# Kernel optimization log

Measured on AMD Instinct MI355X. Metric: run time of the kernel, lower is better.

The kernel has to match this reference:

```python
import jax, jax.numpy as jnp
import numpy as np
from jax import lax

P = 8  # DFFN patch_size


def _ln(x, w, b):
    # WithBias LayerNorm over channel dim of NCHW (matches to_3d -> LN(-1) -> to_4d)
    mu = x.mean(1, keepdims=True)
    var = ((x - mu) ** 2).mean(1, keepdims=True)
    return (x - mu) / jnp.sqrt(var + 1e-5) * w[None, :, None, None] + b[None, :, None, None]


def _conv1x1(x, w, b=None):
    y = jnp.einsum('bchw,oc->bohw', x, w)
    if b is not None:
        y = y + b[None, :, None, None]
    return y


def setup_inputs() -> dict:
    key = jax.random.key(0)
    ks = jax.random.split(key, 9)
    B, C, H, W = 2, 64, 96, 96
    hid = C  # ffn_expansion_factor = 1
    s = lambda k, shape, scale=0.05: jax.random.normal(k, shape, jnp.float32) * scale
    return {
        'x': s(ks[0], (B, C, H, W), 1.0),
        'ln1_w': jnp.ones((C,), jnp.float32), 'ln1_b': jnp.zeros((C,), jnp.float32),
        'ln2_w': jnp.ones((C,), jnp.float32), 'ln2_b': jnp.zeros((C,), jnp.float32),
        'q_w': s(ks[1], (C, C)), 'q_b': jnp.zeros((C,), jnp.float32),
        'k_w': s(ks[2], (C, C)), 'k_b': jnp.zeros((C,), jnp.float32),
        'v_w': s(ks[3], (C, C)), 'v_b': jnp.zeros((C,), jnp.float32),
        'fft_w': s(ks[4], (hid, P, P // 2 + 1), 1.0),
        'proj_in_w': s(ks[5], (hid, C)),
        'dw_w': s(ks[6], (hid, 1, 3, 3)),
        'proj_out_w': s(ks[7], (C, hid // 2)),
    }


def reference(x, ln1_w, ln1_b, ln2_w, ln2_b, q_w, q_b, k_w, k_b, v_w, v_b,
              fft_w, proj_in_w, dw_w, proj_out_w):
    B, C, H, W = x.shape
    # --- attention sub-block (unscaled spatial self-attn) ---
    xn = _ln(x, ln1_w, ln1_b)
    q = _conv1x1(xn, q_w, q_b).reshape(B, C, H * W)
    k = _conv1x1(xn, k_w, k_b).reshape(B, C, H * W)
    v = _conv1x1(xn, v_w, v_b).reshape(B, C, H * W)
    attn = jax.nn.softmax(jnp.einsum('bcn,bcm->bnm', q, k), axis=-1)  # [B, HW, HW]
    out = jnp.einsum('bcm,bnm->bcn', v, attn).reshape(B, C, H, W)
    x = x + out
    # --- DFFN sub-block ---
    xn = _ln(x, ln2_w, ln2_b)
    h = _conv1x1(xn, proj_in_w)  # hidden == C (expansion factor 1)
    hid = h.shape[1]
    hb, wb = H // P, W // P
    hp = h.reshape(B, hid, hb, P, wb, P).transpose(0, 2, 4, 1, 3, 5)  # [B,hb,wb,hid,P,P]
    hf = jnp.fft.rfft2(hp) * fft_w  # real learned spectral filter
    hp = jnp.fft.irfft2(hf, s=(P, P))
    h = hp.transpose(0, 3, 1, 4, 2, 5).reshape(B, hid, H, W)
    h = lax.conv_general_dilated(h, dw_w, (1, 1), ((1, 1), (1, 1)),
                                 feature_group_count=hid,
                                 dimension_numbers=('NCHW', 'OIHW', 'NCHW'))
    h1, h2 = jnp.split(h, 2, axis=1)
    h = jax.nn.gelu(h1, approximate=False) * h2  # torch F.gelu is exact erf
    return x + _conv1x1(h, proj_out_w)
```

## Files before the change

### kernel.cpp

```cpp
#include <hip/hip_runtime.h>
#include <hip/hip_bf16.h>
#include <math.h>

#define CH 64
#define NPOS 9216
#define NTOT 18432
#define NSPLIT 12
#define TILES_PER_SPLIT 12
#define LOG2E 1.4426950408889634f

typedef short bf16x8 __attribute__((ext_vector_type(8)));
typedef short bf16x4 __attribute__((ext_vector_type(4)));
typedef float f32x4 __attribute__((ext_vector_type(4)));
typedef int   i32x4 __attribute__((ext_vector_type(4)));
typedef int   i32x2 __attribute__((ext_vector_type(2)));
typedef unsigned int u32;

__device__ __forceinline__ float bf2f(short s) {
  unsigned int u = ((unsigned int)(unsigned short)s) << 16;
  return __builtin_bit_cast(float, u);
}
__device__ __forceinline__ short f2bf(float f) {
  unsigned int u = __builtin_bit_cast(unsigned int, f);
  unsigned int r = (u + 0x7fffu + ((u >> 16) & 1u)) >> 16;
  return (short)r;
}
__device__ __forceinline__ float gelu_exact(float x) {
  return 0.5f * x * (1.f + erff(x * 0.70710678118654752440f));
}


__global__ __launch_bounds__(256) void k_ln_qkv(
    const float* __restrict__ x, const float* __restrict__ ln1w, const float* __restrict__ ln1b,
    const float* __restrict__ qw, const float* __restrict__ qb,
    const float* __restrict__ kw, const float* __restrict__ kb,
    const float* __restrict__ vw, const float* __restrict__ vb,
    short* __restrict__ Qg, short* __restrict__ Kg, short* __restrict__ Vgt) {
  __shared__ float s1a[256], s2a[256];
  __shared__ __align__(16) short xn[32 * 72];
  int t = threadIdx.x;
  int w8 = t >> 5;
  int p = t & 31;
  int q0 = blockIdx.x * 32;
  int q = q0 + p;
  int b = q / NPOS;
  int nn = q0 % NPOS;
  int n = q % NPOS;

  const float* xb = x + (size_t)b * CH * NPOS + n;
  float xr[8];
  float s1 = 0.f, s2 = 0.f;
#pragma unroll
  for (int cl = 0; cl < 8; ++cl) {
    float v = xb[(size_t)(w8 * 8 + cl) * NPOS];
    xr[cl] = v;
    s1 += v;
    s2 += v * v;
  }
  s1a[w8 * 32 + p] = s1;
  s2a[w8 * 32 + p] = s2;
  __syncthreads();
  float mu = 0.f, m2 = 0.f;
#pragma unroll
  for (int ww = 0; ww < 8; ++ww) { mu += s1a[ww * 32 + p]; m2 += s2a[ww * 32 + p]; }
  mu *= (1.f / 64.f);
  float var = m2 * (1.f / 64.f) - mu * mu;
  float rstd = rsqrtf(var + 1e-5f);
  {
    u32* xw = (u32*)xn;
#pragma unroll
    for (int j2 = 0; j2 < 4; ++j2) {
      int cl = 2 * j2, c = w8 * 8 + cl;
      float y0 = (xr[cl] - mu) * rstd * ln1w[c] + ln1b[c];
      float y1 = (xr[cl + 1] - mu) * rstd * ln1w[c + 1] + ln1b[c + 1];
      u32 pk = ((u32)(unsigned short)f2bf(y1) << 16) | (u32)(unsigned short)f2bf(y0);
      xw[p * 36 + w8 * 4 + j2] = pk;
    }
  }
  __syncthreads();
  int lane = t & 63;
  int L = lane & 15, quad = lane >> 4;
  int cs = t >> 6;
  bf16x8 b0[2], b1[2];
#pragma unroll
  for (int ps = 0; ps < 2; ++ps) {
    b0[ps] = *(const bf16x8*)(xn + (ps * 16 + L) * 72 + quad * 8);
    b1[ps] = *(const bf16x8*)(xn + (ps * 16 + L) * 72 + 32 + quad * 8);
  }
#pragma unroll
  for (int m = 0; m < 3; ++m) {
    const float* wsrc = (m == 0) ? qw : (m == 1) ? kw : vw;
    const float* bsrc = (m == 0) ? qb : (m == 1) ? kb : vb;
    bf16x8 a0, a1;
    {
      const float* wr = wsrc + (cs * 16 + L) * 64 + quad * 8;
#pragma unroll
      for (int j = 0; j < 8; ++j) { a0[j] = f2bf(wr[j]); a1[j] = f2bf(wr[32 + j]); }
    }
    float bi[4];
#pragma unroll
    for (int i = 0; i < 4; ++i) bi[i] = bsrc[cs * 16 + quad * 4 + i];
#pragma unroll
    for (int ps = 0; ps < 2; ++ps) {
      f32x4 acc = {bi[0], bi[1], bi[2], bi[3]};
      acc = __builtin_amdgcn_mfma_f32_16x16x32_bf16(a0, b0[ps], acc, 0, 0, 0);
      acc = __builtin_amdgcn_mfma_f32_16x16x32_bf16(a1, b1[ps], acc, 0, 0, 0);
      int idx = b * NPOS + nn + ps * 16 + L;
      if (m == 0) {
#pragma unroll
        for (int i = 0; i < 4; ++i)
          Qg[(size_t)idx * 64 + cs * 16 + quad * 4 + i] = f2bf(acc[i]);
      } else if (m == 1) {
#pragma unroll
        for (int i = 0; i < 4; ++i)
          Kg[(size_t)idx * 64 + cs * 16 + quad * 4 + i] = f2bf(acc[i] * LOG2E);
      } else {
#pragma unroll
        for (int i = 0; i < 4; ++i)
          Vgt[(size_t)(cs * 16 + quad * 4 + i) * NTOT + idx] = f2bf(acc[i]);
      }
    }
  }
}

#define LDPK 80
#define LDP  72
__global__ __launch_bounds__(512) void k_attn(
    const short* __restrict__ Qg, const short* __restrict__ Kg, const short* __restrict__ Vgt,
    u32* __restrict__ PoT, float* __restrict__ Pl) {
  __shared__ __align__(16) short Kt[2][64 * LDPK];
  __shared__ __align__(16) short Vt[2][64 * LDP];
  int b = blockIdx.y;
  int n0 = blockIdx.x * 256;
  int ks = blockIdx.z;
  int tid = threadIdx.x;
  int w = tid >> 6, lane = tid & 63;
  int L = lane & 15, quad = lane >> 4;

  bf16x8 qa[2][2];
#pragma unroll
  for (int qt = 0; qt < 2; ++qt) {
    const short* qb_ = Qg + ((size_t)(b * NPOS + n0 + w * 32 + qt * 16 + L)) * 64;
    qa[qt][0] = *(const bf16x8*)(qb_ + quad * 8);
    qa[qt][1] = *(const bf16x8*)(qb_ + 32 + quad * 8);
  }

  f32x4 o[2][4];
#pragma unroll
  for (int qt = 0; qt < 2; ++qt)
#pragma unroll
    for (int nb = 0; nb < 4; ++nb) o[qt][nb] = (f32x4){0.f, 0.f, 0.f, 0.f};
  float rl[2] = {0.f, 0.f};

  int ck = tid & 7, rk = tid >> 3;
  int c8 = tid & 7, dr = tid >> 3;
  int vslot = (c8 >> 2) * 32 + (c8 & 1) * 16 + ((c8 >> 1) & 1) * 4;
  i32x4 kr, vr;
  {
    int kt = ks * TILES_PER_SPLIT;
    kr = ((const i32x4*)(Kg + ((size_t)(b * NPOS + kt * 64)) * 64))[tid];
    vr = *(const i32x4*)(Vgt + (size_t)b * NPOS + kt * 64 + c8 * 8 + (size_t)dr * NTOT);
    ((i32x4*)Kt[0])[rk * 10 + ck] = kr;
    short* vrow = Vt[0] + dr * LDP + vslot;
    *(i32x2*)(vrow) = (i32x2){vr[0], vr[1]};
    *(i32x2*)(vrow + 8) = (i32x2){vr[2], vr[3]};
  }

  for (int t = 0; t < TILES_PER_SPLIT; ++t) {
    int cur = t & 1;
    if (t + 1 < TILES_PER_SPLIT) {
      int kt = ks * TILES_PER_SPLIT + t + 1;
      kr = ((const i32x4*)(Kg + ((size_t)(b * NPOS + kt * 64)) * 64))[tid];
      vr = *(const i32x4*)(Vgt + (size_t)b * NPOS + kt * 64 + c8 * 8 + (size_t)dr * NTOT);
    }
    __syncthreads();

    const i32x4* kt4 = (const i32x4*)Kt[cur];
    const short* vt = Vt[cur];
    auto compute_win = [&](int kp) {
      u32 pw0[4], pw1[4];
#pragma unroll
      for (int h = 0; h < 2; ++h) {
        int kti = kp * 2 + h;
        bf16x8 kf0 = __builtin_bit_cast(bf16x8, kt4[(kti * 16 + L) * 10 + quad]);
        bf16x8 kf1 = __builtin_bit_cast(bf16x8, kt4[(kti * 16 + L) * 10 + 4 + quad]);
#pragma unroll
        for (int qt = 0; qt < 2; ++qt) {
          f32x4 st = {0.f, 0.f, 0.f, 0.f};
          st = __builtin_amdgcn_mfma_f32_16x16x32_bf16(kf0, qa[qt][0], st, 0, 0, 0);
          st = __builtin_amdgcn_mfma_f32_16x16x32_bf16(kf1, qa[qt][1], st, 0, 0, 0);
          float p0 = __builtin_amdgcn_exp2f(st[0]);
          float p1 = __builtin_amdgcn_exp2f(st[1]);
          float p2 = __builtin_amdgcn_exp2f(st[2]);
          float p3 = __builtin_amdgcn_exp2f(st[3]);
          rl[qt] += (p0 + p1) + (p2 + p3);
          u32 lo = __builtin_amdgcn_perm(__builtin_bit_cast(u32, p1), __builtin_bit_cast(u32, p0), 0x07060302u);
          u32 hi = __builtin_amdgcn_perm(__builtin_bit_cast(u32, p3), __builtin_bit_cast(u32, p2), 0x07060302u);
          if (qt == 0) { pw0[h * 2] = lo; pw0[h * 2 + 1] = hi; }
          else         { pw1[h * 2] = lo; pw1[h * 2 + 1] = hi; }
        }
      }
      i32x4 pq0 = {(int)pw0[0], (int)pw0[1], (int)pw0[2], (int)pw0[3]};
      i32x4 pq1 = {(int)pw1[0], (int)pw1[1], (int)pw1[2], (int)pw1[3]};
      bf16x8 pp0 = __builtin_bit_cast(bf16x8, pq0);
      bf16x8 pp1 = __builtin_bit_cast(bf16x8, pq1);
#pragma unroll
      for (int nb = 0; nb < 4; ++nb) {
        bf16x8 va8 = *(const bf16x8*)(vt + (nb * 16 + L) * LDP + kp * 32 + quad * 8);
        o[0][nb] = __builtin_amdgcn_mfma_f32_16x16x32_bf16(va8, pp0, o[0][nb], 0, 0, 0);
        o[1][nb] = __builtin_amdgcn_mfma_f32_16x16x32_bf16(va8, pp1, o[1][nb], 0, 0, 0);
      }
    };

    __builtin_amdgcn_s_setprio(1);
    compute_win(0);
    __builtin_amdgcn_s_setprio(0);

    if (t + 1 < TILES_PER_SPLIT) {
      int nxt = 1 - cur;
      ((i32x4*)Kt[nxt])[rk * 10 + ck] = kr;
      short* vrow = Vt[nxt] + dr * LDP + vslot;
      *(i32x2*)(vrow) = (i32x2){vr[0], vr[1]};
      *(i32x2*)(vrow + 8) = (i32x2){vr[2], vr[3]};
    }

    __builtin_amdgcn_s_setprio(1);
    compute_win(1);
    __builtin_amdgcn_s_setprio(0);
  }

#pragma unroll
  for (int qt = 0; qt < 2; ++qt) {
    rl[qt] += __shfl_xor(rl[qt], 16);
    rl[qt] += __shfl_xor(rl[qt], 32);
  }

#pragma unroll
  for (int qt = 0; qt < 2; ++qt) {
    int qg = b * NPOS + n0 + w * 32 + qt * 16 + L;
#pragma unroll
    for (int nb = 0; nb < 4; ++nb)
#pragma unroll
      for (int ip = 0; ip < 2; ++ip) {
        u32 pk = ((u32)(unsigned short)f2bf(o[qt][nb][2 * ip + 1]) << 16) |
                 (u32)(unsigned short)f2bf(o[qt][nb][2 * ip]);
        int d32 = nb * 8 + quad * 2 + ip;
        PoT[((size_t)(ks * 32 + d32)) * NTOT + qg] = pk;
      }
    if (quad == 0) Pl[(size_t)ks * NTOT + qg] = rl[qt];
  }
}

__global__ __launch_bounds__(256) void k_res_ln2_proj(
    const float* __restrict__ x, const u32* __restrict__ PoT, const float* __restrict__ Pl,
    const float* __restrict__ ln2w, const float* __restrict__ ln2b,
    const float* __restrict__ piw,
    float* __restrict__ X2, float* __restrict__ Hbuf) {
  __shared__ float s1a[32 * 32], s2a[32 * 32];
  __shared__ float inva[32], mua[32], rsa[32];
  __shared__ __align__(16) short xn[32 * 72];
  int t = threadIdx.x;
  int q0 = blockIdx.x * 32;
  int b = q0 / NPOS;
  int nn = q0 % NPOS;

  if (t < 32) {
    float ls = 0.f;
#pragma unroll
    for (int s = 0; s < NSPLIT; ++s) ls += Pl[(size_t)s * NTOT + q0 + t];
    inva[t] = 1.f / ls;
  }
  __syncthreads();

  int rho = t >> 3;
  int p4 = (t & 7) * 4;
  int c0 = rho * 2;

  float aL[4] = {0.f, 0.f, 0.f, 0.f}, aH[4] = {0.f, 0.f, 0.f, 0.f};
#pragma unroll
  for (int s = 0; s < NSPLIT; ++s) {
    i32x4 v = *(const i32x4*)(PoT + (size_t)(s * 32 + rho) * NTOT + q0 + p4);
#pragma unroll
    for (int i = 0; i < 4; ++i) {
      u32 u = (u32)v[i];
      aL[i] += __builtin_bit_cast(float, u << 16);
      aH[i] += __builtin_bit_cast(float, u & 0xffff0000u);
    }
  }
  f32x4 x0 = *(const f32x4*)(x + (size_t)b * CH * NPOS + (size_t)c0 * NPOS + nn + p4);
  f32x4 x1 = *(const f32x4*)(x + (size_t)b * CH * NPOS + (size_t)(c0 + 1) * NPOS + nn + p4);
  float v0[4], v1[4];
  f32x4 ps1, ps2;
#pragma unroll
  for (int i = 0; i < 4; ++i) {
    float iv = inva[p4 + i];
    v0[i] = x0[i] + aL[i] * iv;
    v1[i] = x1[i] + aH[i] * iv;
    ps1[i] = v0[i] + v1[i];
    ps2[i] = v0[i] * v0[i] + v1[i] * v1[i];
  }
  *(f32x4*)&s1a[rho * 32 + p4] = ps1;
  *(f32x4*)&s2a[rho * 32 + p4] = ps2;
  {
    float* xo = X2 + (size_t)b * CH * NPOS + nn + p4;
    *(f32x4*)(xo + (size_t)c0 * NPOS) = (f32x4){v0[0], v0[1], v0[2], v0[3]};
    *(f32x4*)(xo + (size_t)(c0 + 1) * NPOS) = (f32x4){v1[0], v1[1], v1[2], v1[3]};
  }
  __syncthreads();
  if (t < 32) {
    float m = 0.f, m2 = 0.f;
#pragma unroll
    for (int r = 0; r < 32; ++r) { m += s1a[r * 32 + t]; m2 += s2a[r * 32 + t]; }
    m *= (1.f / 64.f);
    float var = m2 * (1.f / 64.f) - m * m;
    mua[t] = m;
    rsa[t] = rsqrtf(var + 1e-5f);
  }
  __syncthreads();
  {
    u32* xw = (u32*)xn;
    float w0 = ln2w[c0], w1 = ln2w[c0 + 1];
    float bb0 = ln2b[c0], bb1 = ln2b[c0 + 1];
#pragma unroll
    for (int i = 0; i < 4; ++i) {
      int p = p4 + i;
      float mu = mua[p], rs = rsa[p];
      float y0 = (v0[i] - mu) * rs * w0 + bb0;
      float y1 = (v1[i] - mu) * rs * w1 + bb1;
      xw[p * 36 + rho] = ((u32)(unsigned short)f2bf(y1) << 16) | (u32)(unsigned short)f2bf(y0);
    }
  }
  __syncthreads();
  int lane = t & 63;
  int L = lane & 15, quad = lane >> 4;
  int cs = t >> 6;
  bf16x8 a0, a1;
  {
    const float* wr = piw + (cs * 16 + L) * 64 + quad * 8;
#pragma unroll
    for (int j = 0; j < 8; ++j) { a0[j] = f2bf(wr[j]); a1[j] = f2bf(wr[32 + j]); }
  }
  float* hb = Hbuf + (size_t)b * CH * NPOS + nn;
#pragma unroll
  for (int ps = 0; ps < 2; ++ps) {
    bf16x8 b0 = *(const bf16x8*)(xn + (ps * 16 + L) * 72 + quad * 8);
    bf16x8 b1 = *(const bf16x8*)(xn + (ps * 16 + L) * 72 + 32 + quad * 8);
    f32x4 acc = {0.f, 0.f, 0.f, 0.f};
    acc = __builtin_amdgcn_mfma_f32_16x16x32_bf16(a0, b0, acc, 0, 0, 0);
    acc = __builtin_amdgcn_mfma_f32_16x16x32_bf16(a1, b1, acc, 0, 0, 0);
#pragma unroll
    for (int i = 0; i < 4; ++i)
      hb[(size_t)(cs * 16 + quad * 4 + i) * NPOS + ps * 16 + L] = acc[i];
  }
}

#define LDB 100
__global__ __launch_bounds__(192) void k_conv(
    float* __restrict__ Hbuf, const float* __restrict__ fftw) {
  __shared__ __align__(16) float band[2][8 * LDB];
  __shared__ float kl[64];
  int c = blockIdx.y, b = blockIdx.z;
  int t = threadIdx.x;
  int g = t / 96, tt = t % 96;
  int hb = blockIdx.x * 2 + g;
  float* base = Hbuf + (size_t)(b * CH + c) * NPOS + hb * 8 * 96;
  if (t < 64) {
    int dp = t >> 3, dq = t & 7;
    const float r = 0.70710678118654752440f;
    const float CO[8] = {1.f, r, 0.f, -r, -1.f, -r, 0.f, r};
    const float* wc = fftw + c * 40;
    float acc = 0.f;
#pragma unroll
    for (int u = 0; u < 8; ++u) {
#pragma unroll
      for (int v = 0; v < 8; ++v) {
        float wv = (v <= 4) ? wc[u * 5 + v] : wc[((8 - u) & 7) * 5 + (8 - v)];
        acc += wv * CO[(u * dp + v * dq) & 7];
      }
    }
    kl[t] = acc * (1.f / 64.f);
  }
  {
    int sr = tt / 12, sc = (tt % 12) * 8;
    f32x4 a = *(const f32x4*)(base + sr * 96 + sc);
    f32x4 d = *(const f32x4*)(base + sr * 96 + sc + 4);
    *(f32x4*)&band[g][sr * LDB + sc] = a;
    *(f32x4*)&band[g][sr * LDB + sc + 4] = d;
  }
  __syncthreads();
  int p = tt / 12, wb = tt % 12;
  float out[8] = {0.f, 0.f, 0.f, 0.f, 0.f, 0.f, 0.f, 0.f};
#pragma unroll
  for (int dp = 0; dp < 8; ++dp) {
    int rr = (p - dp) & 7;
    f32x4 a = *(const f32x4*)&band[g][rr * LDB + wb * 8];
    f32x4 d = *(const f32x4*)&band[g][rr * LDB + wb * 8 + 4];
    float v[8] = {a[0], a[1], a[2], a[3], d[0], d[1], d[2], d[3]};
    const float* krow = &kl[dp * 8];
#pragma unroll
    for (int dq = 0; dq < 8; ++dq) {
      float kv = krow[dq];
#pragma unroll
      for (int q = 0; q < 8; ++q) out[q] += kv * v[(q - dq) & 7];
    }
  }
  __syncthreads();
  f32x4 w0 = {out[0], out[1], out[2], out[3]};
  f32x4 w1 = {out[4], out[5], out[6], out[7]};
  *(f32x4*)(base + p * 96 + wb * 8) = w0;
  *(f32x4*)(base + p * 96 + wb * 8 + 4) = w1;
}

__global__ __launch_bounds__(256) void k_dw_gate(
    const float* __restrict__ Hbuf, const float* __restrict__ dww,
    float* __restrict__ G) {
  int cc = blockIdx.y;
  int q4 = (blockIdx.x * 256 + threadIdx.x) * 4;
  int b = q4 / NPOS, n = q4 % NPOS;
  int y = n / 96, x0 = n % 96;
  const float* h1 = Hbuf + (size_t)(b * CH + cc) * NPOS;
  const float* h2 = Hbuf + (size_t)(b * CH + cc + 32) * NPOS;
  float wd1[9], wd2[9];
#pragma unroll
  for (int ki = 0; ki < 9; ++ki) { wd1[ki] = dww[cc * 9 + ki]; wd2[ki] = dww[(cc + 32) * 9 + ki]; }
  f32x4 d1 = {0.f, 0.f, 0.f, 0.f}, d2 = {0.f, 0.f, 0.f, 0.f};
#pragma unroll
  for (int dy = -1; dy <= 1; ++dy) {
    int yy = y + dy;
    if (yy < 0 || yy >= 96) continue;
    const float* r1 = h1 + yy * 96 + x0;
    const float* r2 = h2 + yy * 96 + x0;
    f32x4 c1 = *(const f32x4*)r1;
    f32x4 c2 = *(const f32x4*)r2;
    float l1 = (x0 > 0) ? r1[-1] : 0.f;
    float l2 = (x0 > 0) ? r2[-1] : 0.f;
    float rr1 = (x0 + 4 < 96) ? r1[4] : 0.f;
    float rr2 = (x0 + 4 < 96) ? r2[4] : 0.f;
    int kb = (dy + 1) * 3;
    f32x4 L1 = {l1, c1[0], c1[1], c1[2]};
    f32x4 R1 = {c1[1], c1[2], c1[3], rr1};
    f32x4 L2 = {l2, c2[0], c2[1], c2[2]};
    f32x4 R2 = {c2[1], c2[2], c2[3], rr2};
    d1 += L1 * wd1[kb] + c1 * wd1[kb + 1] + R1 * wd1[kb + 2];
    d2 += L2 * wd2[kb] + c2 * wd2[kb + 1] + R2 * wd2[kb + 2];
  }
  f32x4 gv;
#pragma unroll
  for (int i = 0; i < 4; ++i) gv[i] = gelu_exact(d1[i]) * d2[i];
  *(f32x4*)(G + (size_t)cc * NTOT + q4) = gv;
}

__global__ __launch_bounds__(256) void k_proj_out(
    const float* __restrict__ G, const float* __restrict__ poww,
    const float* __restrict__ X2, float* __restrict__ out) {
  int og = blockIdx.y;
  int q4 = (blockIdx.x * 256 + threadIdx.x) * 4;
  int b = q4 / NPOS, n = q4 % NPOS;
  const float* xr = X2 + (size_t)b * CH * NPOS + n;
  float* ob = out + (size_t)b * CH * NPOS + n;
  f32x4 acc[4];
#pragma unroll
  for (int j = 0; j < 4; ++j)
    acc[j] = *(const f32x4*)(xr + (size_t)(og * 4 + j) * NPOS);
#pragma unroll
  for (int cg = 0; cg < 32; ++cg) {
    f32x4 gv = *(const f32x4*)(G + (size_t)cg * NTOT + q4);
#pragma unroll
    for (int j = 0; j < 4; ++j)
      acc[j] += poww[(og * 4 + j) * 32 + cg] * gv;
  }
#pragma unroll
  for (int j = 0; j < 4; ++j)
    *(f32x4*)(ob + (size_t)(og * 4 + j) * NPOS) = acc[j];
}

extern "C" void kernel_launch(void* const* d_in, const int* in_sizes, int n_in,
                              void* d_out, int out_size, void* d_ws, size_t ws_size,
                              hipStream_t stream) {
  const float* x    = (const float*)d_in[0];
  const float* ln1w = (const float*)d_in[1];
  const float* ln1b = (const float*)d_in[2];
  const float* ln2w = (const float*)d_in[3];
  const float* ln2b = (const float*)d_in[4];
  const float* qw   = (const float*)d_in[5];
  const float* qb   = (const float*)d_in[6];
  const float* kw   = (const float*)d_in[7];
  const float* kb   = (const float*)d_in[8];
  const float* vw   = (const float*)d_in[9];
  const float* vb   = (const float*)d_in[10];
  const float* fftw = (const float*)d_in[11];
  const float* piw  = (const float*)d_in[12];
  const float* dww  = (const float*)d_in[13];
  const float* poww = (const float*)d_in[14];

  short* Qg  = (short*)d_ws;
  short* Kg  = Qg + (size_t)NTOT * 64;
  short* Vgt = Kg + (size_t)NTOT * 64;
  u32*   PoT = (u32*)(Vgt + (size_t)NTOT * 64);
  float* Pl  = (float*)(PoT + (size_t)NSPLIT * 32 * NTOT);
  float* X2  = Pl + (size_t)NSPLIT * NTOT;
  float* Hbuf = X2 + (size_t)NTOT * 64;
  float* G   = Hbuf + (size_t)NTOT * 64;

  k_ln_qkv<<<dim3(576), 256, 0, stream>>>(x, ln1w, ln1b, qw, qb, kw, kb, vw, vb, Qg, Kg, Vgt);
  k_attn<<<dim3(36, 2, NSPLIT), 512, 0, stream>>>(Qg, Kg, Vgt, PoT, Pl);
  k_res_ln2_proj<<<dim3(576), 256, 0, stream>>>(x, PoT, Pl, ln2w, ln2b, piw, X2, Hbuf);
  k_conv<<<dim3(6, 64, 2), 192, 0, stream>>>(Hbuf, fftw);
  k_dw_gate<<<dim3(18, 32), 256, 0, stream>>>(Hbuf, dww, G);
  k_proj_out<<<dim3(18, 16), 256, 0, stream>>>(G, poww, X2, (float*)d_out);
}
```

Before: 164.5 us.

## Double attention block to 1024 threads, split K/V staging, retune split count

The attention kernel now processes 512 queries per block with 1024 threads, so each staged K/V tile in shared memory is reused by twice as many waves. Staging is split by thread half: the first 512 threads load K and the rest load V, which halves the global loads and register staging per thread. The key dimension is re-split into 16 chunks of 9 tiles instead of 12 of 12, which changes the grid and the number of partial results the next kernel merges. The larger launch bound caps registers per thread and may cause spills or lower scheduling flexibility, and each block spends more time at barriers.

New measurement: 176.3 us. +7.1%, slower.

```diff
diff --git a/kernel.cpp b/kernel.cpp
--- a/kernel.cpp
+++ b/kernel.cpp
@@ -5,8 +5,8 @@
 #define CH 64
 #define NPOS 9216
 #define NTOT 18432
-#define NSPLIT 12
-#define TILES_PER_SPLIT 12
+#define NSPLIT 16
+#define TILES_PER_SPLIT 9
 #define LOG2E 1.4426950408889634f
 
 typedef short bf16x8 __attribute__((ext_vector_type(8)));
@@ -125,13 +125,13 @@
 
 #define LDPK 80
 #define LDP  72
-__global__ __launch_bounds__(512) void k_attn(
+__global__ __launch_bounds__(1024) void k_attn(
     const short* __restrict__ Qg, const short* __restrict__ Kg, const short* __restrict__ Vgt,
     u32* __restrict__ PoT, float* __restrict__ Pl) {
   __shared__ __align__(16) short Kt[2][64 * LDPK];
   __shared__ __align__(16) short Vt[2][64 * LDP];
   int b = blockIdx.y;
-  int n0 = blockIdx.x * 256;
+  int n0 = blockIdx.x * 512;
   int ks = blockIdx.z;
   int tid = threadIdx.x;
   int w = tid >> 6, lane = tid & 63;
@@ -152,26 +152,33 @@
     for (int nb = 0; nb < 4; ++nb) o[qt][nb] = (f32x4){0.f, 0.f, 0.f, 0.f};
   float rl[2] = {0.f, 0.f};
 
-  int ck = tid & 7, rk = tid >> 3;
-  int c8 = tid & 7, dr = tid >> 3;
+  int stid = tid & 511;
+  bool isK = tid < 512;
+  int ck = stid & 7, rk = stid >> 3;
+  int c8 = stid & 7, dr = stid >> 3;
   int vslot = (c8 >> 2) * 32 + (c8 & 1) * 16 + ((c8 >> 1) & 1) * 4;
-  i32x4 kr, vr;
+  i32x4 sr;
   {
     int kt = ks * TILES_PER_SPLIT;
-    kr = ((const i32x4*)(Kg + ((size_t)(b * NPOS + kt * 64)) * 64))[tid];
-    vr = *(const i32x4*)(Vgt + (size_t)b * NPOS + kt * 64 + c8 * 8 + (size_t)dr * NTOT);
-    ((i32x4*)Kt[0])[rk * 10 + ck] = kr;
-    short* vrow = Vt[0] + dr * LDP + vslot;
-    *(i32x2*)(vrow) = (i32x2){vr[0], vr[1]};
-    *(i32x2*)(vrow + 8) = (i32x2){vr[2], vr[3]};
+    if (isK) {
+      sr = ((const i32x4*)(Kg + ((size_t)(b * NPOS + kt * 64)) * 64))[stid];
+      ((i32x4*)Kt[0])[rk * 10 + ck] = sr;
+    } else {
+      sr = *(const i32x4*)(Vgt + (size_t)b * NPOS + kt * 64 + c8 * 8 + (size_t)dr * NTOT);
+      short* vrow = Vt[0] + dr * LDP + vslot;
+      *(i32x2*)(vrow) = (i32x2){sr[0], sr[1]};
+      *(i32x2*)(vrow + 8) = (i32x2){sr[2], sr[3]};
+    }
   }
 
   for (int t = 0; t < TILES_PER_SPLIT; ++t) {
     int cur = t & 1;
     if (t + 1 < TILES_PER_SPLIT) {
       int kt = ks * TILES_PER_SPLIT + t + 1;
-      kr = ((const i32x4*)(Kg + ((size_t)(b * NPOS + kt * 64)) * 64))[tid];
-      vr = *(const i32x4*)(Vgt + (size_t)b * NPOS + kt * 64 + c8 * 8 + (size_t)dr * NTOT);
+      if (isK)
+        sr = ((const i32x4*)(Kg + ((size_t)(b * NPOS + kt * 64)) * 64))[stid];
+      else
+        sr = *(const i32x4*)(Vgt + (size_t)b * NPOS + kt * 64 + c8 * 8 + (size_t)dr * NTOT);
     }
     __syncthreads();
 
@@ -218,10 +225,13 @@
 
     if (t + 1 < TILES_PER_SPLIT) {
       int nxt = 1 - cur;
-      ((i32x4*)Kt[nxt])[rk * 10 + ck] = kr;
-      short* vrow = Vt[nxt] + dr * LDP + vslot;
-      *(i32x2*)(vrow) = (i32x2){vr[0], vr[1]};
-      *(i32x2*)(vrow + 8) = (i32x2){vr[2], vr[3]};
+      if (isK) {
+        ((i32x4*)Kt[nxt])[rk * 10 + ck] = sr;
+      } else {
+        short* vrow = Vt[nxt] + dr * LDP + vslot;
+        *(i32x2*)(vrow) = (i32x2){sr[0], sr[1]};
+        *(i32x2*)(vrow + 8) = (i32x2){sr[2], sr[3]};
+      }
     }
 
     __builtin_amdgcn_s_setprio(1);
@@ -503,7 +513,7 @@
   float* G   = Hbuf + (size_t)NTOT * 64;
 
   k_ln_qkv<<<dim3(576), 256, 0, stream>>>(x, ln1w, ln1b, qw, qb, kw, kb, vw, vb, Qg, Kg, Vgt);
-  k_attn<<<dim3(36, 2, NSPLIT), 512, 0, stream>>>(Qg, Kg, Vgt, PoT, Pl);
+  k_attn<<<dim3(18, 2, NSPLIT), 1024, 0, stream>>>(Qg, Kg, Vgt, PoT, Pl);
   k_res_ln2_proj<<<dim3(576), 256, 0, stream>>>(x, PoT, Pl, ln2w, ln2b, piw, X2, Hbuf);
   k_conv<<<dim3(6, 64, 2), 192, 0, stream>>>(Hbuf, fftw);
   k_dw_gate<<<dim3(18, 32), 256, 0, stream>>>(Hbuf, dww, G);
```
